# Kernel optimization log

Hardware: AMD Instinct MI355X
Metric: run time of the kernel (lower is better)

Reference implementation:

```python
import jax, jax.numpy as jnp
import numpy as np

P, V, GRID = 64, 6890, 32
V_SUB = 256          # vertex subsample for the SDF-grid proxy
SCALE_FACTOR = 0.2   # forward() default
SDF_BAND = 0.15      # proxy: phi = relu(band - dist_to_surface) >= 0
N_FACES = 13776


def _trilinear(vol, pts):
    """torch grid_sample 3D, mode=bilinear, padding=zeros, align_corners=False.
    vol: [D,H,W]; pts: [...,3] with (x,y,z) in [-1,1] mapping to (W,H,D)."""
    D, H, W = vol.shape
    x = ((pts[..., 0] + 1.0) * W - 1.0) * 0.5
    y = ((pts[..., 1] + 1.0) * H - 1.0) * 0.5
    z = ((pts[..., 2] + 1.0) * D - 1.0) * 0.5
    x0 = jnp.floor(x).astype(jnp.int32); fx = x - x0
    y0 = jnp.floor(y).astype(jnp.int32); fy = y - y0
    z0 = jnp.floor(z).astype(jnp.int32); fz = z - z0

    def corner(xi, yi, zi, w):
        inb = (xi >= 0) & (xi < W) & (yi >= 0) & (yi < H) & (zi >= 0) & (zi < D)
        v = vol[jnp.clip(zi, 0, D - 1), jnp.clip(yi, 0, H - 1), jnp.clip(xi, 0, W - 1)]
        return jnp.where(inb, v, 0.0) * w

    return (corner(x0,     y0,     z0,     (1 - fx) * (1 - fy) * (1 - fz))
          + corner(x0 + 1, y0,     z0,     fx       * (1 - fy) * (1 - fz))
          + corner(x0,     y0 + 1, z0,     (1 - fx) * fy       * (1 - fz))
          + corner(x0 + 1, y0 + 1, z0,     fx       * fy       * (1 - fz))
          + corner(x0,     y0,     z0 + 1, (1 - fx) * (1 - fy) * fz)
          + corner(x0 + 1, y0,     z0 + 1, fx       * (1 - fy) * fz)
          + corner(x0,     y0 + 1, z0 + 1, (1 - fx) * fy       * fz)
          + corner(x0 + 1, y0 + 1, z0 + 1, fx       * fy       * fz))


def _compute_phi(verts_cs):
    """Deterministic non-negative SDF-grid proxy (stands in for the external
    SDF CUDA op; original computes it under no_grad). verts_cs: [P,V,3] in [-1,1].
    Returns phi: [P,GRID,GRID,GRID] (D,H,W indexing)."""
    # cell centers in normalized coords (align_corners=False convention)
    lin = (2.0 * jnp.arange(GRID, dtype=verts_cs.dtype) + 1.0) / GRID - 1.0
    zz, yy, xx = jnp.meshgrid(lin, lin, lin, indexing='ij')
    gp = jnp.stack([xx, yy, zz], axis=-1).reshape(-1, 3)  # [G^3,3] (x,y,z)
    stride = V // V_SUB
    sub = verts_cs[:, ::stride, :][:, :V_SUB]             # [P,V_SUB,3]

    def per_person(v):  # v: [V_SUB,3]
        d2 = jnp.sum((gp[:, None, :] - v[None, :, :]) ** 2, axis=-1)  # [G^3,V_SUB]
        d = jnp.sqrt(jnp.min(d2, axis=-1))
        return jnp.maximum(SDF_BAND - d, 0.0).reshape(GRID, GRID, GRID)

    return jax.lax.map(per_person, sub)  # sequential over people: bounds peak memory


def _forward(vertices, translation):
    sg = jax.lax.stop_gradient
    verts = vertices + translation[:, None, :]                      # [P,V,3]
    n = verts.shape[0]
    bmin = sg(jnp.min(verts, axis=1))                               # [P,3] (no_grad bboxes)
    bmax = sg(jnp.max(verts, axis=1))
    # overlap(i,j) per axis: not (min_i > max_j or min_j > max_i)
    ov = jnp.all((bmin[:, None, :] <= bmax[None, :, :]) &
                 (bmin[None, :, :] <= bmax[:, None, :]), axis=-1)   # [P,P], diag True
    # faithful to original ~filter_isolated_boxes: kept only if overlapping ALL others
    valid = jnp.all(ov, axis=1)                                     # [P]
    nv = jnp.sum(valid.astype(verts.dtype))
    center = (bmin + bmax) * 0.5                                    # [P,3]
    scale = (1.0 + SCALE_FACTOR) * 0.5 * jnp.max(bmax - bmin, axis=-1)  # [P]
    verts_cs = sg((verts - center[:, None, :]) / scale[:, None, None])
    phi = sg(_compute_phi(verts_cs))                                # [P,G,G,G]
    # coordinates of ALL people's vertices in person-i's grid frame: [P,P,V,3]
    loc = (verts[None, :, :, :] - center[:, None, None, :]) / scale[:, None, None, None]
    phi_val = jax.vmap(_trilinear)(phi, loc.reshape(n, n * V, 3)).reshape(n, n, V)
    # pair (i,j) contributes iff both valid and i != j (weights[i]=0 in the loop)
    pair_w = (valid[:, None] & valid[None, :] & ~jnp.eye(n, dtype=bool)).astype(verts.dtype)
    denom = jnp.maximum(nv, 1.0) ** 2
    return jnp.sum(pair_w * jnp.sum(phi_val, axis=-1)) / denom


def setup_inputs() -> dict:
    key = jax.random.key(0)
    k1, k2, k3 = jax.random.split(key, 3)
    vertices = jax.random.normal(k1, (P, V, 3), dtype=jnp.float32) * 0.2
    translation = jax.random.uniform(k2, (P, 3), dtype=jnp.float32, minval=-0.3, maxval=0.3)
    faces = jax.random.randint(k3, (N_FACES, 3), 0, V, dtype=jnp.int32)
    return {"vertices": vertices, "translation": translation, "faces": faces}


def reference(vertices, translation, faces):
    # faces only feed the external SDF op (replaced by the phi proxy); unused here
    return _forward(vertices, translation)
```

## Files before the change

### kernel.cpp

```cpp
#include <hip/hip_runtime.h>


#define NP 64
#define NVERT 6890
#define NV3 (NVERT*3)
#define GRD 32
#define QDIM 34
#define QPLANE (QDIM*QDIM)
#define QVOL (QDIM*QPLANE)
#define VSUB 256
#define VSTRIDE 26
#define BAND 0.15f
#define PHI_SCALE 64.0f
#define INV_PHI_SCALE 0.015625f
#define LDS_BYTES (QVOL*2 + 64)
#define SAMPLE_BLOCKS (8*NP)

typedef float floatx2 __attribute__((ext_vector_type(2)));

__device__ __forceinline__ float wave_min(float v) {
  #pragma unroll
  for (int off = 32; off > 0; off >>= 1) v = fminf(v, __shfl_down(v, off));
  return v;
}
__device__ __forceinline__ float wave_max(float v) {
  #pragma unroll
  for (int off = 32; off > 0; off >>= 1) v = fmaxf(v, __shfl_down(v, off));
  return v;
}
__device__ __forceinline__ float wave_sum(float v) {
  #pragma unroll
  for (int off = 32; off > 0; off >>= 1) v += __shfl_down(v, off);
  return v;
}

__global__ __launch_bounds__(256) void k_soa_bounds(
    const float* __restrict__ verts, const float* __restrict__ trans,
    float* __restrict__ vertsT, float* __restrict__ bbox,
    float* __restrict__ accp, unsigned int* __restrict__ donep) {
  int p = blockIdx.x;
  if (p == 0 && threadIdx.x == 0) { accp[0] = 0.0f; donep[0] = 0u; }
  const float* vp = verts + (size_t)p * NV3;
  float tx = trans[p*3+0], ty = trans[p*3+1], tz = trans[p*3+2];
  float* o0 = vertsT + (size_t)(p*3+0) * NVERT;
  float* o1 = vertsT + (size_t)(p*3+1) * NVERT;
  float* o2 = vertsT + (size_t)(p*3+2) * NVERT;
  float mnx=1e30f, mny=1e30f, mnz=1e30f, mxx=-1e30f, mxy=-1e30f, mxz=-1e30f;
  for (int v = threadIdx.x; v < NVERT; v += blockDim.x) {
    float x = vp[v*3+0]+tx, y = vp[v*3+1]+ty, z = vp[v*3+2]+tz;
    o0[v] = x; o1[v] = y; o2[v] = z;
    mnx=fminf(mnx,x); mny=fminf(mny,y); mnz=fminf(mnz,z);
    mxx=fmaxf(mxx,x); mxy=fmaxf(mxy,y); mxz=fmaxf(mxz,z);
  }
  mnx=wave_min(mnx); mny=wave_min(mny); mnz=wave_min(mnz);
  mxx=wave_max(mxx); mxy=wave_max(mxy); mxz=wave_max(mxz);
  __shared__ float s[4][6];
  int wave = threadIdx.x >> 6, lane = threadIdx.x & 63;
  if (lane == 0) {
    s[wave][0]=mnx; s[wave][1]=mny; s[wave][2]=mnz;
    s[wave][3]=mxx; s[wave][4]=mxy; s[wave][5]=mxz;
  }
  __syncthreads();
  if (threadIdx.x == 0) {
    float a0=s[0][0],a1=s[0][1],a2=s[0][2],b0=s[0][3],b1=s[0][4],b2=s[0][5];
    for (int w = 1; w < 4; ++w) {
      a0=fminf(a0,s[w][0]); a1=fminf(a1,s[w][1]); a2=fminf(a2,s[w][2]);
      b0=fmaxf(b0,s[w][3]); b1=fmaxf(b1,s[w][4]); b2=fmaxf(b2,s[w][5]);
    }
    bbox[p*3+0]=a0; bbox[p*3+1]=a1; bbox[p*3+2]=a2;
    bbox[192+p*3+0]=b0; bbox[192+p*3+1]=b1; bbox[192+p*3+2]=b2;
  }
}

__global__ __launch_bounds__(1024) void k_phi(
    const float* __restrict__ verts, const float* __restrict__ trans,
    const float* __restrict__ bbox, unsigned short* __restrict__ pairs,
    float* __restrict__ centerg,
    float* __restrict__ validg, int* __restrict__ jlistg,
    int* __restrict__ jcountg, float* __restrict__ nvg) {
  int p = blockIdx.x >> 2;
  int zq = blockIdx.x & 3;
  int tid = threadIdx.x;
  int x = tid & 31, y = tid >> 5;

  __shared__ float kv[VSUB][3];
  __shared__ float phib[8][32][32];
  __shared__ int nkeep;

  const float inv = 1.0f / (float)GRD;
  if (tid == 0) nkeep = 0;
  __syncthreads();

  float bx0 = bbox[p*3+0], by0 = bbox[p*3+1], bz0 = bbox[p*3+2];
  float bx1 = bbox[192+p*3+0], by1 = bbox[192+p*3+1], bz1 = bbox[192+p*3+2];
  float cx = 0.5f*(bx0+bx1), cy = 0.5f*(by0+by1), cz = 0.5f*(bz0+bz1);
  float ext = fmaxf(bx1-bx0, fmaxf(by1-by0, bz1-bz0));
  float is = 1.0f / (0.6f * ext);

  if (zq == 0 && tid == 0) {
    centerg[p*4+0] = cx; centerg[p*4+1] = cy; centerg[p*4+2] = cz;
    centerg[p*4+3] = is * 16.0f;
  }
  if (blockIdx.x == 0 && tid < 64) {
    bool valid = true;
    for (int j = 0; j < NP; ++j) {
      bool ov = true;
      #pragma unroll
      for (int c = 0; c < 3; ++c)
        ov = ov && (bbox[tid*3+c] <= bbox[192+j*3+c]) &&
                   (bbox[j*3+c] <= bbox[192+tid*3+c]);
      valid = valid && ov;
    }
    unsigned long long mm = __ballot(valid);
    if (valid) {
      int pos = (int)__popcll(mm & ((1ull << tid) - 1ull));
      jlistg[pos] = tid;
    }
    validg[tid] = valid ? 1.0f : 0.0f;
    if (tid == 0) {
      jcountg[0] = (int)__popcll(mm);
      nvg[0] = (float)__popcll(mm);
    }
  }

  if (tid < VSUB) {
    int v = tid * VSTRIDE;
    const float* vp = verts + (size_t)p * NV3 + (size_t)v * 3;
    float X = (vp[0] + trans[p*3+0] - cx) * is;
    float Y = (vp[1] + trans[p*3+1] - cy) * is;
    float Z = (vp[2] + trans[p*3+2] - cz) * is;
    float zlo = (2.0f*(zq*8)     + 1.0f) * inv - 1.0f;
    float zhi = (2.0f*(zq*8 + 7) + 1.0f) * inv - 1.0f;
    float dz = fmaxf(fmaxf(zlo - Z, Z - zhi), 0.0f);
    if (dz < BAND) {
      int idx = atomicAdd(&nkeep, 1);
      kv[idx][0] = X; kv[idx][1] = Y; kv[idx][2] = Z;
    }
  }
  __syncthreads();
  int nk = nkeep;

  float gx = (2.0f*x + 1.0f) * inv - 1.0f;
  float gy = (2.0f*y + 1.0f) * inv - 1.0f;
  float gz[8];
  #pragma unroll
  for (int k = 0; k < 8; ++k) gz[k] = (2.0f*(zq*8+k) + 1.0f) * inv - 1.0f;

  float d2[8];
  #pragma unroll
  for (int k = 0; k < 8; ++k) d2[k] = 1e30f;

  int w = tid >> 6;
  float ylo = (4.0f*w + 1.0f) * inv - 1.0f;
  float yhi = (4.0f*w + 3.0f) * inv - 1.0f;

  for (int v = 0; v < nk; ++v) {
    float Y = kv[v][1];
    if (fmaxf(ylo - Y, Y - yhi) >= BAND) continue;
    float dx = gx - kv[v][0];
    float dy = gy - Y;
    float vz = kv[v][2];
    float r2 = fmaf(dy, dy, dx*dx);
    #pragma unroll
    for (int k = 0; k < 8; ++k) {
      float dz = gz[k] - vz;
      d2[k] = fminf(d2[k], fmaf(dz, dz, r2));
    }
  }
  #pragma unroll
  for (int k = 0; k < 8; ++k)
    phib[k][y][x] = fmaxf(BAND - sqrtf(d2[k]), 0.0f) * PHI_SCALE;
  __syncthreads();

  unsigned short* qp = pairs + (size_t)p * QVOL;
  for (int idx = tid; idx < QPLANE; idx += 1024) {
    int iy = idx / QDIM, ix = idx % QDIM;
    int gyy = iy - 1, gxx = ix - 1;
    bool gyok = (unsigned)gyy < 32u;
    bool aok = gyok && ((unsigned)gxx < 32u);
    bool bok = gyok && ((unsigned)ix  < 32u);
    int ya = gyok ? gyy : 0;
    int xa = aok ? gxx : 0;
    int xb = bok ? ix : 0;
    #pragma unroll
    for (int k = 0; k < 8; ++k) {
      float a = aok ? phib[k][ya][xa] : 0.0f;
      float b = bok ? phib[k][ya][xb] : 0.0f;
      int pk = __builtin_amdgcn_cvt_pk_fp8_f32(a, b, 0, false);
      qp[(zq*8 + k + 1)*QPLANE + idx] = (unsigned short)(pk & 0xffff);
    }
    if (zq == 0) qp[idx] = 0;
    if (zq == 3) qp[33*QPLANE + idx] = 0;
  }
}

__device__ __forceinline__ float qsample(const unsigned short* q,
                                         float X, float Y, float Z) {
  X = fminf(fmaxf(X, 0.0f), 33.99f);
  Y = fminf(fmaxf(Y, 0.0f), 32.999f);
  Z = fminf(fmaxf(Z, 0.0f), 32.999f);
  float xf = floorf(X), yf = floorf(Y), zf = floorf(Z);
  float fx = X - xf, fy = Y - yf, fz = Z - zf;
  int e = ((int)zf * QDIM + (int)yf) * QDIM + (int)xf;
  unsigned int w00 = q[e];
  unsigned int w10 = q[e + QDIM];
  unsigned int w01 = q[e + QPLANE];
  unsigned int w11 = q[e + QPLANE + QDIM];
  floatx2 c00 = __builtin_amdgcn_cvt_pk_f32_fp8((int)w00, false);
  floatx2 c10 = __builtin_amdgcn_cvt_pk_f32_fp8((int)w10, false);
  floatx2 c01 = __builtin_amdgcn_cvt_pk_f32_fp8((int)w01, false);
  floatx2 c11 = __builtin_amdgcn_cvt_pk_f32_fp8((int)w11, false);
  float u00 = fmaf(fx, c00.y - c00.x, c00.x);
  float u10 = fmaf(fx, c10.y - c10.x, c10.x);
  float u01 = fmaf(fx, c01.y - c01.x, c01.x);
  float u11 = fmaf(fx, c11.y - c11.x, c11.x);
  float a0 = fmaf(fy, u10 - u00, u00);
  float a1 = fmaf(fy, u11 - u01, u01);
  return fmaf(fz, a1 - a0, a0);
}

__global__ __launch_bounds__(896, 7) void k_sample(
    const float* __restrict__ vertsT, const float* __restrict__ centerg,
    const float* __restrict__ validg, const unsigned short* __restrict__ pairs,
    const int* __restrict__ jlistg, const int* __restrict__ jcountg,
    const float* __restrict__ nvg, float* __restrict__ accp,
    unsigned int* __restrict__ donep, float* __restrict__ out) {
  extern __shared__ unsigned char smem[];
  const unsigned short* sq = (const unsigned short*)smem;
  float* red = (float*)(smem + (size_t)QVOL * 2);

  int i = blockIdx.y;
  int tid = threadIdx.x;
  int njl = jcountg[0];

  if (validg[i] != 0.0f) {
    {
      const uint4* src = (const uint4*)(pairs + (size_t)i * QVOL);
      uint4* dst = (uint4*)smem;
      for (int t = tid; t < QVOL/8; t += 896) dst[t] = src[t];
    }
    __syncthreads();

    int v = blockIdx.x * 896 + tid;
    bool ok = v < NVERT;
    int vc = ok ? v : 0;
    float s16 = centerg[i*4+3];
    float bx = fmaf(-centerg[i*4+0], s16, 16.5f) + (ok ? 0.0f : 1e9f);
    float by = fmaf(-centerg[i*4+1], s16, 16.5f);
    float bz = fmaf(-centerg[i*4+2], s16, 16.5f);

    float acc = 0.0f;
    #pragma unroll 2
    for (int t = 0; t < njl; ++t) {
      int jj = jlistg[t];
      if (jj == i) continue;
      const float* p0 = vertsT + (size_t)(jj*3) * NVERT;
      float X = fmaf(p0[vc],         s16, bx);
      float Y = fmaf(p0[NVERT+vc],   s16, by);
      float Z = fmaf(p0[2*NVERT+vc], s16, bz);
      acc += qsample(sq, X, Y, Z);
    }

    acc = wave_sum(acc);
    int wv = tid >> 6, lane = tid & 63;
    if (lane == 0) red[wv] = acc;
    __syncthreads();
    if (tid == 0) {
      float tot = 0.0f;
      #pragma unroll
      for (int w = 0; w < 14; ++w) tot += red[w];
      atomicAdd(accp, tot * INV_PHI_SCALE);
    }
  }

  if (tid == 0) {
    __threadfence();
    unsigned int old = atomicAdd(donep, 1u);
    if (old == SAMPLE_BLOCKS - 1) {
      float nv = fmaxf(nvg[0], 1.0f);
      float loss = atomicAdd(accp, 0.0f);
      out[0] = loss / (nv * nv);
    }
  }
}

extern "C" void kernel_launch(void* const* d_in, const int* in_sizes, int n_in,
                              void* d_out, int out_size, void* d_ws, size_t ws_size,
                              hipStream_t stream) {
  const float* verts = (const float*)d_in[0];
  const float* trans = (const float*)d_in[1];
  float* out = (float*)d_out;

  unsigned short* pairs = (unsigned short*)d_ws;
  float* vertsT    = (float*)((unsigned char*)d_ws + (size_t)NP * QVOL * 2);
  float* bbox      = vertsT + (size_t)NP * NV3;
  float* centerg   = bbox + 384;
  float* validg    = centerg + NP*4;
  float* nvg       = validg + NP;
  float* accp      = nvg + 1;
  unsigned int* donep = (unsigned int*)(accp + 1);
  int* jlistg      = (int*)(donep + 1);
  int* jcountg     = jlistg + NP;

  hipFuncSetAttribute((const void*)k_sample,
                      hipFuncAttributeMaxDynamicSharedMemorySize, LDS_BYTES);

  k_soa_bounds<<<NP, 256, 0, stream>>>(verts, trans, vertsT, bbox, accp, donep);
  k_phi<<<NP*4, 1024, 0, stream>>>(verts, trans, bbox, pairs, centerg,
                                   validg, jlistg, jcountg, nvg);
  k_sample<<<dim3(8, NP), 896, LDS_BYTES, stream>>>(vertsT, centerg, validg,
                                                    pairs, jlistg, jcountg,
                                                    nvg, accp, donep, out);
}
```

Measured before the change: 106.8 us.

## Fuse bounds pass into phi kernel and split grid into eight z-slabs

Removes the separate SoA/bounding-box kernel. Each phi block now recomputes its own person's bbox redundantly, writes an eighth of the transposed vertices, and the last-arriving block (found via an atomic counter) computes the validity list. The phi grid doubles to 512 blocks with 4 z-slices each, which means more parallelism and less register pressure. In exchange each block re-reads the full vertex set, and a memset replaces the in-kernel counter init.

```diff
diff --git a/kernel.cpp b/kernel.cpp
--- a/kernel.cpp
+++ b/kernel.cpp
@@ -4,6 +4,7 @@
 #define NP 64
 #define NVERT 6890
 #define NV3 (NVERT*3)
+#define QCH8 862
 #define GRD 32
 #define QDIM 34
 #define QPLANE (QDIM*QDIM)
@@ -14,6 +15,7 @@
 #define PHI_SCALE 64.0f
 #define INV_PHI_SCALE 0.015625f
 #define LDS_BYTES (QVOL*2 + 64)
+#define PHI_BLOCKS (NP*8)
 #define SAMPLE_BLOCKS (8*NP)
 
 typedef float floatx2 __attribute__((ext_vector_type(2)));
@@ -34,74 +36,69 @@
   return v;
 }
 
-__global__ __launch_bounds__(256) void k_soa_bounds(
+__global__ __launch_bounds__(1024) void k_phi(
     const float* __restrict__ verts, const float* __restrict__ trans,
-    float* __restrict__ vertsT, float* __restrict__ bbox,
-    float* __restrict__ accp, unsigned int* __restrict__ donep) {
-  int p = blockIdx.x;
-  if (p == 0 && threadIdx.x == 0) { accp[0] = 0.0f; donep[0] = 0u; }
+    unsigned short* __restrict__ pairs, float* __restrict__ vertsT,
+    float* __restrict__ bbox, float* __restrict__ centerg,
+    float* __restrict__ validg, int* __restrict__ jlistg,
+    int* __restrict__ jcountg, float* __restrict__ nvg,
+    unsigned int* __restrict__ phidone) {
+  int p = blockIdx.x >> 3;
+  int zq = blockIdx.x & 7;
+  int tid = threadIdx.x;
+  int x = tid & 31, y = tid >> 5;
+
+  __shared__ float kv[VSUB][3];
+  __shared__ float phib[4][32][32];
+  __shared__ float s[16][6];
+  __shared__ float bbf[6];
+  __shared__ int nkeep;
+  __shared__ int amLast;
+
   const float* vp = verts + (size_t)p * NV3;
   float tx = trans[p*3+0], ty = trans[p*3+1], tz = trans[p*3+2];
-  float* o0 = vertsT + (size_t)(p*3+0) * NVERT;
-  float* o1 = vertsT + (size_t)(p*3+1) * NVERT;
-  float* o2 = vertsT + (size_t)(p*3+2) * NVERT;
   float mnx=1e30f, mny=1e30f, mnz=1e30f, mxx=-1e30f, mxy=-1e30f, mxz=-1e30f;
-  for (int v = threadIdx.x; v < NVERT; v += blockDim.x) {
-    float x = vp[v*3+0]+tx, y = vp[v*3+1]+ty, z = vp[v*3+2]+tz;
-    o0[v] = x; o1[v] = y; o2[v] = z;
-    mnx=fminf(mnx,x); mny=fminf(mny,y); mnz=fminf(mnz,z);
-    mxx=fmaxf(mxx,x); mxy=fmaxf(mxy,y); mxz=fmaxf(mxz,z);
+  for (int v = tid; v < NVERT; v += 1024) {
+    float xx = vp[v*3+0]+tx, yy = vp[v*3+1]+ty, zz = vp[v*3+2]+tz;
+    mnx=fminf(mnx,xx); mny=fminf(mny,yy); mnz=fminf(mnz,zz);
+    mxx=fmaxf(mxx,xx); mxy=fmaxf(mxy,yy); mxz=fmaxf(mxz,zz);
+  }
+  {
+    float* o0 = vertsT + (size_t)(p*3+0) * NVERT;
+    float* o1 = vertsT + (size_t)(p*3+1) * NVERT;
+    float* o2 = vertsT + (size_t)(p*3+2) * NVERT;
+    int q0 = zq * QCH8;
+    int q1 = q0 + QCH8; if (q1 > NVERT) q1 = NVERT;
+    for (int v = q0 + tid; v < q1; v += 1024) {
+      o0[v] = vp[v*3+0]+tx; o1[v] = vp[v*3+1]+ty; o2[v] = vp[v*3+2]+tz;
+    }
   }
   mnx=wave_min(mnx); mny=wave_min(mny); mnz=wave_min(mnz);
   mxx=wave_max(mxx); mxy=wave_max(mxy); mxz=wave_max(mxz);
-  __shared__ float s[4][6];
-  int wave = threadIdx.x >> 6, lane = threadIdx.x & 63;
+  int wave = tid >> 6, lane = tid & 63;
   if (lane == 0) {
     s[wave][0]=mnx; s[wave][1]=mny; s[wave][2]=mnz;
     s[wave][3]=mxx; s[wave][4]=mxy; s[wave][5]=mxz;
   }
   __syncthreads();
-  if (threadIdx.x == 0) {
+  if (tid == 0) {
     float a0=s[0][0],a1=s[0][1],a2=s[0][2],b0=s[0][3],b1=s[0][4],b2=s[0][5];
-    for (int w = 1; w < 4; ++w) {
+    for (int w = 1; w < 16; ++w) {
       a0=fminf(a0,s[w][0]); a1=fminf(a1,s[w][1]); a2=fminf(a2,s[w][2]);
       b0=fmaxf(b0,s[w][3]); b1=fmaxf(b1,s[w][4]); b2=fmaxf(b2,s[w][5]);
     }
+    bbf[0]=a0; bbf[1]=a1; bbf[2]=a2; bbf[3]=b0; bbf[4]=b1; bbf[5]=b2;
     bbox[p*3+0]=a0; bbox[p*3+1]=a1; bbox[p*3+2]=a2;
     bbox[192+p*3+0]=b0; bbox[192+p*3+1]=b1; bbox[192+p*3+2]=b2;
-  }
-}
-
-__global__ __launch_bounds__(1024) void k_phi(
-    const float* __restrict__ verts, const float* __restrict__ trans,
-    const float* __restrict__ bbox, unsigned short* __restrict__ pairs,
-    float* __restrict__ centerg,
-    float* __restrict__ validg, int* __restrict__ jlistg,
-    int* __restrict__ jcountg, float* __restrict__ nvg) {
-  int p = blockIdx.x >> 2;
-  int zq = blockIdx.x & 3;
-  int tid = threadIdx.x;
-  int x = tid & 31, y = tid >> 5;
-
-  __shared__ float kv[VSUB][3];
-  __shared__ float phib[8][32][32];
-  __shared__ int nkeep;
-
-  const float inv = 1.0f / (float)GRD;
-  if (tid == 0) nkeep = 0;
+    nkeep = 0;
+    __threadfence();
+    unsigned int old = atomicAdd(phidone, 1u);
+    amLast = (old == PHI_BLOCKS - 1) ? 1 : 0;
+  }
   __syncthreads();
 
-  float bx0 = bbox[p*3+0], by0 = bbox[p*3+1], bz0 = bbox[p*3+2];
-  float bx1 = bbox[192+p*3+0], by1 = bbox[192+p*3+1], bz1 = bbox[192+p*3+2];
-  float cx = 0.5f*(bx0+bx1), cy = 0.5f*(by0+by1), cz = 0.5f*(bz0+bz1);
-  float ext = fmaxf(bx1-bx0, fmaxf(by1-by0, bz1-bz0));
-  float is = 1.0f / (0.6f * ext);
-
-  if (zq == 0 && tid == 0) {
-    centerg[p*4+0] = cx; centerg[p*4+1] = cy; centerg[p*4+2] = cz;
-    centerg[p*4+3] = is * 16.0f;
-  }
-  if (blockIdx.x == 0 && tid < 64) {
+  if (amLast && tid < 64) {
+    __threadfence();
     bool valid = true;
     for (int j = 0; j < NP; ++j) {
       bool ov = true;
@@ -123,14 +120,25 @@
     }
   }
 
+  float cx = 0.5f*(bbf[0]+bbf[3]), cy = 0.5f*(bbf[1]+bbf[4]);
+  float cz = 0.5f*(bbf[2]+bbf[5]);
+  float ext = fmaxf(bbf[3]-bbf[0], fmaxf(bbf[4]-bbf[1], bbf[5]-bbf[2]));
+  float is = 1.0f / (0.6f * ext);
+  const float inv = 1.0f / (float)GRD;
+
+  if (zq == 0 && tid == 0) {
+    centerg[p*4+0] = cx; centerg[p*4+1] = cy; centerg[p*4+2] = cz;
+    centerg[p*4+3] = is * 16.0f;
+  }
+
   if (tid < VSUB) {
     int v = tid * VSTRIDE;
-    const float* vp = verts + (size_t)p * NV3 + (size_t)v * 3;
-    float X = (vp[0] + trans[p*3+0] - cx) * is;
-    float Y = (vp[1] + trans[p*3+1] - cy) * is;
-    float Z = (vp[2] + trans[p*3+2] - cz) * is;
-    float zlo = (2.0f*(zq*8)     + 1.0f) * inv - 1.0f;
-    float zhi = (2.0f*(zq*8 + 7) + 1.0f) * inv - 1.0f;
+    const float* vv = vp + (size_t)v * 3;
+    float X = (vv[0] + tx - cx) * is;
+    float Y = (vv[1] + ty - cy) * is;
+    float Z = (vv[2] + tz - cz) * is;
+    float zlo = (2.0f*(zq*4)     + 1.0f) * inv - 1.0f;
+    float zhi = (2.0f*(zq*4 + 3) + 1.0f) * inv - 1.0f;
     float dz = fmaxf(fmaxf(zlo - Z, Z - zhi), 0.0f);
     if (dz < BAND) {
       int idx = atomicAdd(&nkeep, 1);
@@ -142,13 +150,13 @@
 
   float gx = (2.0f*x + 1.0f) * inv - 1.0f;
   float gy = (2.0f*y + 1.0f) * inv - 1.0f;
-  float gz[8];
-  #pragma unroll
-  for (int k = 0; k < 8; ++k) gz[k] = (2.0f*(zq*8+k) + 1.0f) * inv - 1.0f;
-
-  float d2[8];
-  #pragma unroll
-  for (int k = 0; k < 8; ++k) d2[k] = 1e30f;
+  float gz[4];
+  #pragma unroll
+  for (int k = 0; k < 4; ++k) gz[k] = (2.0f*(zq*4+k) + 1.0f) * inv - 1.0f;
+
+  float d2[4];
+  #pragma unroll
+  for (int k = 0; k < 4; ++k) d2[k] = 1e30f;
 
   int w = tid >> 6;
   float ylo = (4.0f*w + 1.0f) * inv - 1.0f;
@@ -162,13 +170,13 @@
     float vz = kv[v][2];
     float r2 = fmaf(dy, dy, dx*dx);
     #pragma unroll
-    for (int k = 0; k < 8; ++k) {
+    for (int k = 0; k < 4; ++k) {
       float dz = gz[k] - vz;
       d2[k] = fminf(d2[k], fmaf(dz, dz, r2));
     }
   }
   #pragma unroll
-  for (int k = 0; k < 8; ++k)
+  for (int k = 0; k < 4; ++k)
     phib[k][y][x] = fmaxf(BAND - sqrtf(d2[k]), 0.0f) * PHI_SCALE;
   __syncthreads();
 
@@ -183,14 +191,14 @@
     int xa = aok ? gxx : 0;
     int xb = bok ? ix : 0;
     #pragma unroll
-    for (int k = 0; k < 8; ++k) {
+    for (int k = 0; k < 4; ++k) {
       float a = aok ? phib[k][ya][xa] : 0.0f;
       float b = bok ? phib[k][ya][xb] : 0.0f;
       int pk = __builtin_amdgcn_cvt_pk_fp8_f32(a, b, 0, false);
-      qp[(zq*8 + k + 1)*QPLANE + idx] = (unsigned short)(pk & 0xffff);
+      qp[(zq*4 + k + 1)*QPLANE + idx] = (unsigned short)(pk & 0xffff);
     }
     if (zq == 0) qp[idx] = 0;
-    if (zq == 3) qp[33*QPLANE + idx] = 0;
+    if (zq == 7) qp[33*QPLANE + idx] = 0;
   }
 }
 
@@ -298,16 +306,18 @@
   float* validg    = centerg + NP*4;
   float* nvg       = validg + NP;
   float* accp      = nvg + 1;
-  unsigned int* donep = (unsigned int*)(accp + 1);
-  int* jlistg      = (int*)(donep + 1);
+  unsigned int* donep   = (unsigned int*)(accp + 1);
+  unsigned int* phidone = donep + 1;
+  int* jlistg      = (int*)(phidone + 1);
   int* jcountg     = jlistg + NP;
 
   hipFuncSetAttribute((const void*)k_sample,
                       hipFuncAttributeMaxDynamicSharedMemorySize, LDS_BYTES);
 
-  k_soa_bounds<<<NP, 256, 0, stream>>>(verts, trans, vertsT, bbox, accp, donep);
-  k_phi<<<NP*4, 1024, 0, stream>>>(verts, trans, bbox, pairs, centerg,
-                                   validg, jlistg, jcountg, nvg);
+  hipMemsetAsync(accp, 0, 12, stream);
+  k_phi<<<PHI_BLOCKS, 1024, 0, stream>>>(verts, trans, pairs, vertsT, bbox,
+                                         centerg, validg, jlistg, jcountg,
+                                         nvg, phidone);
   k_sample<<<dim3(8, NP), 896, LDS_BYTES, stream>>>(vertsT, centerg, validg,
                                                     pairs, jlistg, jcountg,
                                                     nvg, accp, donep, out);
```

Result: slower. 123.8 us (+16.0%).
